# Kernel optimization log

Measured on AMD Instinct MI355X. Metric: run time of the kernel, lower is better.

## Reference

```python
import jax, jax.numpy as jnp
import numpy as np
from jax import lax

KERNELS_DESC = [{"weight": 0.9, "xy": 6.0, "image": 0.1}, {"weight": 0.1, "xy": 6.0}]
RADIUS = 5
DIAM = 2 * RADIUS + 1


def _unfold(t, d, r):
    # torch F.unfold with zero padding r, stride 1 -> [n, c, d*d, h, w]
    n, c, h, w = t.shape
    p = lax.conv_general_dilated_patches(t, (d, d), (1, 1), [(r, r), (r, r)])
    return p.reshape(n, c, d * d, h, w)


def setup_inputs() -> dict:
    key = jax.random.key(0)
    k1, k2 = jax.random.split(key)
    N, H, W = 2, 256, 256
    return {
        "x": jax.random.uniform(k1, (N, 3, H, W), dtype=jnp.float32),
        "y": jax.random.normal(k2, (N, H, W), dtype=jnp.float32),
        "mask_src": jnp.ones((N, 1, H, W), dtype=jnp.float32),
        "mask_dst": jnp.ones((N, 1, H, W), dtype=jnp.float32),
    }


def reference(x, y, mask_src, mask_dst):
    N, _, H, W = x.shape
    d, r = DIAM, RADIUS
    center = r * d + r  # flat index of window center

    y_hat = jax.nn.sigmoid(y)
    y2 = jnp.stack([1.0 - y_hat, y_hat], axis=1)  # [N,2,H,W]

    xx = jnp.broadcast_to(jnp.arange(W, dtype=jnp.float32)[None, None, None, :], (N, 1, H, W))
    yy = jnp.broadcast_to(jnp.arange(H, dtype=jnp.float32)[None, None, :, None], (N, 1, H, W))
    xy = jnp.concatenate([xx, yy], axis=1)  # [N,2,H,W]

    kernels = jnp.zeros((N, 1, d * d, H, W), dtype=x.dtype)
    for desc in KERNELS_DESC:
        feats = []
        for modality, sigma in desc.items():
            if modality == "weight":
                continue
            f = xy if modality == "xy" else x
            feats.append(f / sigma)
        feats = jnp.concatenate(feats, axis=1)  # [N,c,H,W]
        patches = _unfold(feats, d, r)          # [N,c,d2,H,W]
        diff = patches - feats[:, :, None]      # center-pixel difference
        k = jnp.exp(-0.5 * jnp.sum(diff * diff, axis=1, keepdims=True))  # [N,1,d2,H,W]
        k = k.at[:, :, center].set(0.0)
        kernels = kernels + desc["weight"] * k

    # mask_src: denom taken BEFORE binarization (matches torch in-place order)
    denom = jnp.maximum(jnp.sum(mask_src), 1.0)
    ms = jnp.where(jnp.isnan(mask_src), 0.0, mask_src)
    ms = jnp.where(ms < 1.0, 0.0, ms)
    kernels = kernels * _unfold(ms, d, r)

    # mask_dst: denom taken AFTER binarization, overrides mask_src denom
    md = jnp.where(jnp.isnan(mask_dst), 0.0, mask_dst)
    md = jnp.where(md < 1.0, 0.0, md)
    denom = jnp.maximum(jnp.sum(md), 1.0)
    kernels = kernels * md[:, :, None]  # [N,1,1,H,W] broadcasts over d2

    yu = _unfold(y2, d, r)                   # [N,2,d2,H,W]
    prod = jnp.sum(kernels * yu, axis=2)     # [N,2,H,W]
    loss = (jnp.sum(kernels) - jnp.sum(prod * y2)) / denom
    return loss
```

## Files before the change

### kernel.cpp

```cpp
#include <hip/hip_runtime.h>
#include <math.h>

#define RADIUS 5
#define DIAM   11

constexpr int TILE = 16;
constexpr int LT   = TILE + 2 * RADIUS;
constexpr int NOFF = 60;

__device__ __forceinline__ float binarize(float v) {
    return (isnan(v) || v < 1.0f) ? 0.0f : v;
}

__global__ __launch_bounds__(256) void crf_main(
    const float* __restrict__ x,
    const float* __restrict__ y,
    const float* __restrict__ msrc,
    const float* __restrict__ mdst,
    float2* __restrict__ partial,
    int H, int W)
{
    __shared__ float4 sP[LT][LT];
    __shared__ float2 sM[LT][LT];
    __shared__ float  sExy[NOFF];
    __shared__ float  wRedA[4], wRedB[4];

    const int n   = blockIdx.z;
    const int ti0 = blockIdx.y * TILE;
    const int tj0 = blockIdx.x * TILE;
    const int tid = threadIdx.y * TILE + threadIdx.x;

    if (tid < NOFF) {
        int di, dj;
        if (tid < 5) { di = 0; dj = tid + 1; }
        else         { di = (tid - 5) / DIAM + 1; dj = (tid - 5) % DIAM - RADIUS; }
        sExy[tid] = __expf(-(float)(di * di + dj * dj) * (1.0f / 72.0f));
    }

    const long long planeHW = (long long)H * W;
    const float* xn  = x    + (long long)n * 3 * planeHW;
    const float* yn  = y    + (long long)n * planeHW;
    const float* msn = msrc + (long long)n * planeHW;
    const float* mdn = mdst + (long long)n * planeHW;

    for (int idx = tid; idx < LT * LT; idx += 256) {
        int li = idx / LT, lj = idx % LT;
        int gi = ti0 - RADIUS + li;
        int gj = tj0 - RADIUS + lj;
        float4 P = make_float4(0.f, 0.f, 0.f, 0.f);
        float2 M = make_float2(0.f, 0.f);
        if (gi >= 0 && gi < H && gj >= 0 && gj < W) {
            long long p = (long long)gi * W + gj;
            P.x = xn[p];
            P.y = xn[planeHW + p];
            P.z = xn[2 * planeHW + p];
            P.w = 1.0f / (1.0f + __expf(-yn[p]));
            M.x = binarize(msn[p]);
            M.y = binarize(mdn[p]);
        }
        sP[li][lj] = P;
        sM[li][lj] = M;
    }
    __syncthreads();

    const int ci = threadIdx.y + RADIUS, cj = threadIdx.x + RADIUS;
    const int gi = ti0 + threadIdx.y,    gj = tj0 + threadIdx.x;
    const bool valid = (gi < H && gj < W);

    float lsum = 0.0f, mdb = 0.0f;
    if (valid) {
        const float4 C  = sP[ci][cj];
        const float2 Mc = sM[ci][cj];
        const float  sc   = C.w;
        const float  c1m2 = 1.0f - 2.0f * sc;
        mdb = Mc.y;

        #pragma unroll
        for (int k = 0; k < NOFF; ++k) {
            int di, dj;
            if (k < 5) { di = 0; dj = k + 1; }
            else       { di = (k - 5) / DIAM + 1; dj = (k - 5) % DIAM - RADIUS; }
            const float4 P = sP[ci + di][cj + dj];
            const float2 M = sM[ci + di][cj + dj];
            float d0 = P.x - C.x, d1 = P.y - C.y, d2 = P.z - C.z;
            float u  = fmaf(d2, d2, fmaf(d1, d1, d0 * d0));
            float e  = __expf(-50.0f * u);
            float w  = sExy[k] * fmaf(0.9f, e, 0.1f);
            float oms = fmaf(P.w, c1m2, sc);
            float pm  = fmaf(Mc.x, M.y, M.x * Mc.y);
            lsum = fmaf(w * oms, pm, lsum);
        }
    }

    float a = lsum, b = mdb;
    #pragma unroll
    for (int off = 32; off > 0; off >>= 1) {
        a += __shfl_down(a, off, 64);
        b += __shfl_down(b, off, 64);
    }
    const int wave = tid >> 6, lane = tid & 63;
    if (lane == 0) { wRedA[wave] = a; wRedB[wave] = b; }
    __syncthreads();
    if (tid == 0) {
        float t1 = wRedA[0] + wRedA[1] + wRedA[2] + wRedA[3];
        float t2 = wRedB[0] + wRedB[1] + wRedB[2] + wRedB[3];
        int bid = (blockIdx.z * gridDim.y + blockIdx.y) * gridDim.x + blockIdx.x;
        partial[bid] = make_float2(t1, t2);
    }
}

__global__ __launch_bounds__(256) void crf_final(
    const float2* __restrict__ partial, int G, float* __restrict__ out)
{
    __shared__ float wRedA[4], wRedB[4];
    float a = 0.f, b = 0.f;
    for (int i = threadIdx.x; i < G; i += 256) {
        float2 p = partial[i];
        a += p.x; b += p.y;
    }
    #pragma unroll
    for (int off = 32; off > 0; off >>= 1) {
        a += __shfl_down(a, off, 64);
        b += __shfl_down(b, off, 64);
    }
    const int wave = threadIdx.x >> 6, lane = threadIdx.x & 63;
    if (lane == 0) { wRedA[wave] = a; wRedB[wave] = b; }
    __syncthreads();
    if (threadIdx.x == 0) {
        double num   = (double)wRedA[0] + wRedA[1] + wRedA[2] + wRedA[3];
        double denom = (double)wRedB[0] + wRedB[1] + wRedB[2] + wRedB[3];
        if (denom < 1.0) denom = 1.0;
        out[0] = (float)(num / denom);
    }
}

extern "C" void kernel_launch(void* const* d_in, const int* in_sizes, int n_in,
                              void* d_out, int out_size, void* d_ws, size_t ws_size,
                              hipStream_t stream) {
    const float* x  = (const float*)d_in[0];
    const float* yv = (const float*)d_in[1];
    const float* ms = (const float*)d_in[2];
    const float* md = (const float*)d_in[3];
    float* out      = (float*)d_out;
    float2* partial = (float2*)d_ws;

    const int H = 256, W = 256;
    const int N = in_sizes[1] / (H * W);

    dim3 block(TILE, TILE);
    dim3 grid((W + TILE - 1) / TILE, (H + TILE - 1) / TILE, N);
    const int G = grid.x * grid.y * grid.z;

    hipLaunchKernelGGL(crf_main, grid, block, 0, stream, x, yv, ms, md, partial, H, W);
    hipLaunchKernelGGL(crf_final, dim3(1), dim3(256), 0, stream, partial, G, out);
}
```

Measured before the change: 69.15 us.

## Split neighbor offsets across two thread halves and bake spatial weights as constants

Each block now has 512 threads: two threads per pixel, each handling half of the 60 symmetric neighbor offsets, and the per-wave partials are reduced over 8 waves. The spatial Gaussian weights are precomputed at compile time, folded with the 0.9/0.1 mix and used as immediates, which removes the shared-memory table and its setup. This aims to double the parallelism on a small grid (512 blocks) where per-thread serial work dominates. The cost is more threads per block and a larger block-level reduction.

Measured after the change: 75.52 us. +9.2%, slower.

```diff
diff --git a/kernel.cpp b/kernel.cpp
--- a/kernel.cpp
+++ b/kernel.cpp
@@ -7,12 +7,62 @@
 constexpr int TILE = 16;
 constexpr int LT   = TILE + 2 * RADIUS;
 constexpr int NOFF = 60;
+constexpr int HALF_OFF = 30;
+
+constexpr double cexp_small(double x) {
+    double s = 1.0, t = 1.0;
+    for (int i = 1; i <= 22; ++i) { t *= x / (double)i; s += t; }
+    return s;
+}
+
+struct WTab { float c1[NOFF]; float c2[NOFF]; };
+
+constexpr WTab make_wtab() {
+    WTab w{};
+    for (int k = 0; k < NOFF; ++k) {
+        int di, dj;
+        if (k < 5) { di = 0; dj = k + 1; }
+        else       { di = (k - 5) / DIAM + 1; dj = (k - 5) % DIAM - RADIUS; }
+        double e = cexp_small(-(double)(di * di + dj * dj) / 72.0);
+        w.c1[k] = (float)(0.9 * e);
+        w.c2[k] = (float)(0.1 * e);
+    }
+    return w;
+}
+
+constexpr WTab WT = make_wtab();
 
 __device__ __forceinline__ float binarize(float v) {
     return (isnan(v) || v < 1.0f) ? 0.0f : v;
 }
 
-__global__ __launch_bounds__(256) void crf_main(
+template<int K0>
+__device__ __forceinline__ float accum_half(
+    const float4 (*sP)[LT], const float2 (*sM)[LT],
+    int ci, int cj, float4 C, float2 Mc)
+{
+    const float sc   = C.w;
+    const float c1m2 = 1.0f - 2.0f * sc;
+    float lsum = 0.0f;
+    #pragma unroll
+    for (int k = K0; k < K0 + HALF_OFF; ++k) {
+        int di, dj;
+        if (k < 5) { di = 0; dj = k + 1; }
+        else       { di = (k - 5) / DIAM + 1; dj = (k - 5) % DIAM - RADIUS; }
+        const float4 P = sP[ci + di][cj + dj];
+        const float2 M = sM[ci + di][cj + dj];
+        float d0 = P.x - C.x, d1 = P.y - C.y, d2 = P.z - C.z;
+        float u  = fmaf(d2, d2, fmaf(d1, d1, d0 * d0));
+        float e  = __expf(-50.0f * u);
+        float w  = fmaf(WT.c1[k], e, WT.c2[k]);
+        float oms = fmaf(P.w, c1m2, sc);
+        float pm  = fmaf(Mc.x, M.y, M.x * Mc.y);
+        lsum = fmaf(w * oms, pm, lsum);
+    }
+    return lsum;
+}
+
+__global__ __launch_bounds__(512, 4) void crf_main(
     const float* __restrict__ x,
     const float* __restrict__ y,
     const float* __restrict__ msrc,
@@ -22,20 +72,12 @@
 {
     __shared__ float4 sP[LT][LT];
     __shared__ float2 sM[LT][LT];
-    __shared__ float  sExy[NOFF];
-    __shared__ float  wRedA[4], wRedB[4];
+    __shared__ float  wRedA[8], wRedB[8];
 
     const int n   = blockIdx.z;
     const int ti0 = blockIdx.y * TILE;
     const int tj0 = blockIdx.x * TILE;
-    const int tid = threadIdx.y * TILE + threadIdx.x;
-
-    if (tid < NOFF) {
-        int di, dj;
-        if (tid < 5) { di = 0; dj = tid + 1; }
-        else         { di = (tid - 5) / DIAM + 1; dj = (tid - 5) % DIAM - RADIUS; }
-        sExy[tid] = __expf(-(float)(di * di + dj * dj) * (1.0f / 72.0f));
-    }
+    const int tid = (threadIdx.z * TILE + threadIdx.y) * TILE + threadIdx.x;
 
     const long long planeHW = (long long)H * W;
     const float* xn  = x    + (long long)n * 3 * planeHW;
@@ -43,7 +85,7 @@
     const float* msn = msrc + (long long)n * planeHW;
     const float* mdn = mdst + (long long)n * planeHW;
 
-    for (int idx = tid; idx < LT * LT; idx += 256) {
+    for (int idx = tid; idx < LT * LT; idx += 512) {
         int li = idx / LT, lj = idx % LT;
         int gi = ti0 - RADIUS + li;
         int gj = tj0 - RADIUS + lj;
@@ -71,24 +113,11 @@
     if (valid) {
         const float4 C  = sP[ci][cj];
         const float2 Mc = sM[ci][cj];
-        const float  sc   = C.w;
-        const float  c1m2 = 1.0f - 2.0f * sc;
-        mdb = Mc.y;
-
-        #pragma unroll
-        for (int k = 0; k < NOFF; ++k) {
-            int di, dj;
-            if (k < 5) { di = 0; dj = k + 1; }
-            else       { di = (k - 5) / DIAM + 1; dj = (k - 5) % DIAM - RADIUS; }
-            const float4 P = sP[ci + di][cj + dj];
-            const float2 M = sM[ci + di][cj + dj];
-            float d0 = P.x - C.x, d1 = P.y - C.y, d2 = P.z - C.z;
-            float u  = fmaf(d2, d2, fmaf(d1, d1, d0 * d0));
-            float e  = __expf(-50.0f * u);
-            float w  = sExy[k] * fmaf(0.9f, e, 0.1f);
-            float oms = fmaf(P.w, c1m2, sc);
-            float pm  = fmaf(Mc.x, M.y, M.x * Mc.y);
-            lsum = fmaf(w * oms, pm, lsum);
+        if (threadIdx.z == 0) {
+            lsum = accum_half<0>(sP, sM, ci, cj, C, Mc);
+            mdb  = Mc.y;
+        } else {
+            lsum = accum_half<HALF_OFF>(sP, sM, ci, cj, C, Mc);
         }
     }
 
@@ -102,8 +131,9 @@
     if (lane == 0) { wRedA[wave] = a; wRedB[wave] = b; }
     __syncthreads();
     if (tid == 0) {
-        float t1 = wRedA[0] + wRedA[1] + wRedA[2] + wRedA[3];
-        float t2 = wRedB[0] + wRedB[1] + wRedB[2] + wRedB[3];
+        float t1 = 0.f, t2 = 0.f;
+        #pragma unroll
+        for (int wv = 0; wv < 8; ++wv) { t1 += wRedA[wv]; t2 += wRedB[wv]; }
         int bid = (blockIdx.z * gridDim.y + blockIdx.y) * gridDim.x + blockIdx.x;
         partial[bid] = make_float2(t1, t2);
     }
@@ -147,7 +177,7 @@
     const int H = 256, W = 256;
     const int N = in_sizes[1] / (H * W);
 
-    dim3 block(TILE, TILE);
+    dim3 block(TILE, TILE, 2);
     dim3 grid((W + TILE - 1) / TILE, (H + TILE - 1) / TILE, N);
     const int G = grid.x * grid.y * grid.z;
 
```
